# Optimization experiments

Measured on AMD Instinct MI355X. Metric: run time of the kernel, lower is better.

## Reference

```python
import jax, jax.numpy as jnp
import numpy as np

B, D, H, Z, E = 2048, 1024, 1024, 256, 64


def setup_inputs() -> dict:
    key = jax.random.key(0)
    ks = jax.random.split(key, 16)
    s = lambda k, shape, std=0.02: jax.random.normal(k, shape, dtype=jnp.float32) * std
    return {
        "x": jax.random.normal(ks[0], (B, D), dtype=jnp.float32),
        "h0": jax.random.normal(ks[1], (B, H), dtype=jnp.float32),
        "c0": jax.random.normal(ks[2], (B, H), dtype=jnp.float32),
        "hhat0": jax.random.normal(ks[3], (B, Z), dtype=jnp.float32),
        "chat0": jax.random.normal(ks[4], (B, Z), dtype=jnp.float32),
        "hweight": s(ks[5], (Z + H + D, 4 * Z)),
        "hbias": jnp.zeros((4 * Z,), jnp.float32),
        "zweight_h": s(ks[6], (Z, 4 * E), 0.01),
        "zweight_x": s(ks[7], (Z, 4 * E), 0.01),
        "zweight_b": s(ks[8], (Z, 4 * E), 0.01),
        "zbias_h": jnp.ones((4 * E,), jnp.float32),
        "zbias_x": jnp.ones((4 * E,), jnp.float32),
        # stacked in gate order (i, g, f, o), matching the torch cat order
        "dweight_h": jnp.full((4, E, H), 0.1 / E, jnp.float32),
        "dweight_x": jnp.full((4, E, H), 0.1 / E, jnp.float32),
        "dweight_b": s(ks[9], (4, E, H), 0.01),
        "weight": s(ks[10], (H + D, 4 * H)),
        "bias": jnp.zeros((4 * H,), jnp.float32),
    }


def reference(x, h0, c0, hhat0, chat0, hweight, hbias,
              zweight_h, zweight_x, zweight_b, zbias_h, zbias_x,
              dweight_h, dweight_x, dweight_b, weight, bias):
    # ---- hyper LSTM cell ----
    hcat = jnp.concatenate([hhat0, h0, x], axis=1)                 # [B, Z+H+D]
    hg = hcat @ hweight + hbias                                    # [B, 4Z]
    i_h, g_h, f_h, o_h = jnp.split(hg, 4, axis=1)
    chat1 = jax.nn.sigmoid(f_h) * chat0 + jax.nn.sigmoid(i_h) * jnp.tanh(g_h)
    hhat1 = jax.nn.sigmoid(o_h) * jnp.tanh(chat1)                  # [B, Z]

    # ---- embeddings z (gate order i, g, f, o) ----
    z_h = (hhat1 @ zweight_h + zbias_h).reshape(-1, 4, E)          # [B,4,E]
    z_x = (hhat1 @ zweight_x + zbias_x).reshape(-1, 4, E)
    z_b = (hhat1 @ zweight_b).reshape(-1, 4, E)

    # ---- per-gate modulation vectors d_y* : [B,4,H] -> [B,4H] ----
    d_yh = jnp.einsum('bge,geh->bgh', z_h, dweight_h).reshape(-1, 4 * H)
    d_yx = jnp.einsum('bge,geh->bgh', z_x, dweight_x).reshape(-1, 4 * H)
    d_yb = jnp.einsum('bge,geh->bgh', z_b, dweight_b).reshape(-1, 4 * H)

    # ---- main LSTM with hypernetwork modulation ----
    gates = jnp.concatenate([h0, x], axis=1) @ weight              # [B, 4H]
    gates = gates * d_yh * d_yx + d_yb + bias
    i_g, g_g, f_g, o_g = jnp.split(gates, 4, axis=1)
    c1 = jax.nn.sigmoid(f_g) * c0 + jax.nn.sigmoid(i_g) * jnp.tanh(g_g)
    h1 = jax.nn.sigmoid(o_g) * jnp.tanh(c1)
    return (h1, c1, hhat1, chat1)
```

## Files before the change

kernel.cpp:

```cpp
#include <hip/hip_runtime.h>
#include <hip/hip_bf16.h>
#include <math.h>


typedef __attribute__((ext_vector_type(8))) short bf16x8;
typedef __attribute__((ext_vector_type(4))) float f32x4;
typedef unsigned short u16;

__device__ __forceinline__ u16 f2b(float f) {
  union { float f; unsigned u; } v; v.f = f;
  unsigned r = v.u + 0x7fffu + ((v.u >> 16) & 1u);
  return (u16)(r >> 16);
}
__device__ __forceinline__ float b2f(u16 b) {
  union { unsigned u; float f; } v; v.u = ((unsigned)b) << 16; return v.f;
}
__device__ __forceinline__ float sigm(float x) { return 1.f / (1.f + __expf(-x)); }

#define GLL16(gsrc, ldst)                                                      \
  __builtin_amdgcn_global_load_lds(                                            \
      (const __attribute__((address_space(1))) void*)(gsrc),                   \
      (__attribute__((address_space(3))) void*)(ldst), 16, 0, 0)

__global__ void k_prep(const float* __restrict__ hhat0, const float* __restrict__ h0,
                       const float* __restrict__ x, const float* __restrict__ weight,
                       const float* __restrict__ hweight,
                       const float* __restrict__ zw_h, const float* __restrict__ zw_x,
                       const float* __restrict__ zw_b, const float* __restrict__ dw_h,
                       const float* __restrict__ dw_x, const float* __restrict__ dw_b,
                       u16* __restrict__ hcatb, u16* __restrict__ bt,
                       u16* __restrict__ zwT, u16* __restrict__ dwT) {
  __shared__ float tile[32][66];
  int bid = blockIdx.x;
  const int t = threadIdx.x;
  if (bid < 4608) {
    int i = bid * 256 + t;
    int b = i / 576, c4 = i % 576;
    const float* src;
    if (c4 < 64)       src = hhat0 + (long)b * 256 + c4 * 4;
    else if (c4 < 320) src = h0 + (long)b * 1024 + (c4 - 64) * 4;
    else               src = x + (long)b * 1024 + (c4 - 320) * 4;
    float4 v = *(const float4*)src;
    ushort4 o = {f2b(v.x), f2b(v.y), f2b(v.z), f2b(v.w)};
    *(ushort4*)&hcatb[(long)b * 2304 + c4 * 4] = o;
    return;
  }
  bid -= 4608;
  if (bid < 5760) {
    const int n0 = (bid % 160) * 32, k0 = (bid / 160) * 64;
    if (n0 < 4096 && k0 < 256) return;
    const float* src; int C, sc0, sr0;
    if (n0 >= 4096) { src = hweight; C = 1024; sc0 = n0 - 4096; sr0 = k0; }
    else            { src = weight;  C = 4096; sc0 = n0;        sr0 = k0 - 256; }
    #pragma unroll
    for (int p = 0; p < 8; ++p) {
      int c = t & 31, r = (t >> 5) + 8 * p;
      tile[c][r] = src[(long)(sr0 + r) * C + sc0 + c];
    }
    __syncthreads();
    #pragma unroll
    for (int p = 0; p < 2; ++p) {
      int kc = t & 15, cl = (t >> 4) + 16 * p;
      ushort4 o = {f2b(tile[cl][4 * kc]), f2b(tile[cl][4 * kc + 1]),
                   f2b(tile[cl][4 * kc + 2]), f2b(tile[cl][4 * kc + 3])};
      *(ushort4*)&bt[(long)(n0 + cl) * 2304 + k0 + 4 * kc] = o;
    }
    return;
  }
  bid -= 5760;
  const int zi = bid >> 5, bx = bid & 31;
  const float* src; u16* dst; int R, C;
  if (zi < 3) {
    src = (zi == 0) ? zw_h : (zi == 1) ? zw_x : zw_b;
    dst = zwT + (long)zi * 65536; R = 256; C = 256;
  } else {
    int s = zi - 3, tt = s >> 2, g = s & 3;
    src = ((tt == 0) ? dw_h : (tt == 1) ? dw_x : dw_b) + (long)g * 65536;
    dst = dwT + (long)s * 65536; R = 64; C = 1024;
  }
  const int nct = C / 32;
  const int c0 = (bx % nct) * 32, r0 = (bx / nct) * 64;
  #pragma unroll
  for (int p = 0; p < 8; ++p) {
    int c = t & 31, r = (t >> 5) + 8 * p;
    tile[c][r] = src[(long)(r0 + r) * C + c0 + c];
  }
  __syncthreads();
  #pragma unroll
  for (int p = 0; p < 2; ++p) {
    int kc = t & 15, cl = (t >> 4) + 16 * p;
    ushort4 o = {f2b(tile[cl][4 * kc]), f2b(tile[cl][4 * kc + 1]),
                 f2b(tile[cl][4 * kc + 2]), f2b(tile[cl][4 * kc + 3])};
    *(ushort4*)&dst[(long)(c0 + cl) * R + r0 + 4 * kc] = o;
  }
}

__global__ __launch_bounds__(512, 4)
void k_gemm_main(const u16* __restrict__ A, const u16* __restrict__ Bt,
                 float* __restrict__ hgbuf, u16* __restrict__ grawb) {
  constexpr int K = 2304, BK = 32;
  __shared__ __align__(16) u16 sA[128 * BK];
  __shared__ __align__(16) u16 sB[128 * BK];
  const int m0 = blockIdx.y * 128, n0 = blockIdx.x * 128;
  const int kstart = (n0 < 4096) ? 256 : 0;
  const int tid = threadIdx.x, wave = tid >> 6, lane = tid & 63;
  const int quad = lane >> 4, lrow = lane & 15;
  const int wm = (wave >> 2) * 64, wn = (wave & 3) * 32;

  const int sl = tid * 16;
  const int srow = sl >> 6;
  const int sq = (((sl & 63) >> 4) - (srow >> 1)) & 3;
  const long aoff = ((long)(m0 + srow) * K) * 2 + sq * 16;
  const long boff = ((long)(n0 + srow) * K) * 2 + sq * 16;

  const f32x4 vz = {0.f, 0.f, 0.f, 0.f};
  f32x4 acc[4][2];
  #pragma unroll
  for (int i = 0; i < 4; ++i)
    #pragma unroll
    for (int j = 0; j < 2; ++j) acc[i][j] = vz;

  for (int k0 = kstart; k0 < K; k0 += BK) {
    GLL16((const char*)A + aoff + (long)k0 * 2, (char*)sA + wave * 1024);
    GLL16((const char*)Bt + boff + (long)k0 * 2, (char*)sB + wave * 1024);
    __syncthreads();
    bf16x8 af[4], bf[2];
    #pragma unroll
    for (int i = 0; i < 4; ++i) {
      int row = wm + i * 16 + lrow;
      af[i] = *(const bf16x8*)((const char*)sA + row * 64 + (((quad + (row >> 1)) & 3) << 4));
    }
    #pragma unroll
    for (int j = 0; j < 2; ++j) {
      int row = wn + j * 16 + lrow;
      bf[j] = *(const bf16x8*)((const char*)sB + row * 64 + (((quad + (row >> 1)) & 3) << 4));
    }
    #pragma unroll
    for (int i = 0; i < 4; ++i)
      #pragma unroll
      for (int j = 0; j < 2; ++j)
        acc[i][j] = __builtin_amdgcn_mfma_f32_16x16x32_bf16(af[i], bf[j], acc[i][j], 0, 0, 0);
    __syncthreads();
  }
  #pragma unroll
  for (int i = 0; i < 4; ++i) {
    #pragma unroll
    for (int j = 0; j < 2; ++j) {
      #pragma unroll
      for (int r = 0; r < 4; ++r) {
        int row = m0 + wm + i * 16 + quad * 4 + r;
        int col = n0 + wn + j * 16 + lrow;
        float v = acc[i][j][r];
        if (col < 4096) grawb[(long)row * 4096 + col] = f2b(v);
        else            hgbuf[(long)row * 1024 + (col - 4096)] = v;
      }
    }
  }
}

__global__ __launch_bounds__(256, 2)
void k_gemm_z(const u16* __restrict__ A, const u16* __restrict__ Bt,
              const float* __restrict__ zbh, const float* __restrict__ zbx,
              u16* __restrict__ zbout) {
  constexpr int K = 256, BK = 32;
  __shared__ __align__(16) u16 sA[64 * BK];
  __shared__ __align__(16) u16 sB[128 * BK];
  const int m0 = blockIdx.y * 64, n0 = blockIdx.x * 128;
  const int tid = threadIdx.x, wave = tid >> 6, lane = tid & 63;
  const int quad = lane >> 4, lrow = lane & 15;
  const int wm = (wave >> 1) * 32, wn = (wave & 1) * 64;

  const int sl = tid * 16;
  const int arow = sl >> 6;
  const int aq = (((sl & 63) >> 4) - (arow >> 1)) & 3;
  const long aoff = ((long)(m0 + arow) * K) * 2 + aq * 16;

  const f32x4 vz = {0.f, 0.f, 0.f, 0.f};
  f32x4 acc[2][4];
  #pragma unroll
  for (int i = 0; i < 2; ++i)
    #pragma unroll
    for (int j = 0; j < 4; ++j) acc[i][j] = vz;

  for (int k0 = 0; k0 < K; k0 += BK) {
    GLL16((const char*)A + aoff + (long)k0 * 2, (char*)sA + wave * 1024);
    #pragma unroll
    for (int c = 0; c < 2; ++c) {
      int l = c * 4096 + sl;
      int row = l >> 6;
      int q = (((l & 63) >> 4) - (row >> 1)) & 3;
      const char* g = (const char*)Bt + ((long)(n0 + row) * K + k0) * 2 + q * 16;
      GLL16(g, (char*)sB + c * 4096 + wave * 1024);
    }
    __syncthreads();
    bf16x8 af[2], bf[4];
    #pragma unroll
    for (int i = 0; i < 2; ++i) {
      int row = wm + i * 16 + lrow;
      af[i] = *(const bf16x8*)((const char*)sA + row * 64 + (((quad + (row >> 1)) & 3) << 4));
    }
    #pragma unroll
    for (int j = 0; j < 4; ++j) {
      int row = wn + j * 16 + lrow;
      bf[j] = *(const bf16x8*)((const char*)sB + row * 64 + (((quad + (row >> 1)) & 3) << 4));
    }
    #pragma unroll
    for (int i = 0; i < 2; ++i)
      #pragma unroll
      for (int j = 0; j < 4; ++j)
        acc[i][j] = __builtin_amdgcn_mfma_f32_16x16x32_bf16(af[i], bf[j], acc[i][j], 0, 0, 0);
    __syncthreads();
  }
  #pragma unroll
  for (int i = 0; i < 2; ++i) {
    #pragma unroll
    for (int j = 0; j < 4; ++j) {
      #pragma unroll
      for (int r = 0; r < 4; ++r) {
        int row = m0 + wm + i * 16 + quad * 4 + r;
        int col = n0 + wn + j * 16 + lrow;
        float v = acc[i][j][r] + ((col < 256) ? zbh[col] : (col < 512) ? zbx[col - 256] : 0.f);
        zbout[(long)row * 768 + col] = f2b(v);
      }
    }
  }
}

__global__ void k_hyper_act(const float* __restrict__ hgbuf, const float* __restrict__ hbias,
                            const float* __restrict__ chat0,
                            float* __restrict__ chat1, float* __restrict__ hhat1,
                            u16* __restrict__ hhat1b) {
  int idx = blockIdx.x * 256 + threadIdx.x;
  int b = idx >> 8, zc = idx & 255;
  const float* row = hgbuf + (long)b * 1024;
  float ih = row[zc] + hbias[zc];
  float gh = row[256 + zc] + hbias[256 + zc];
  float fh = row[512 + zc] + hbias[512 + zc];
  float oh = row[768 + zc] + hbias[768 + zc];
  float c = sigm(fh) * chat0[idx] + sigm(ih) * tanhf(gh);
  float h = sigm(oh) * tanhf(c);
  chat1[idx] = c;
  hhat1[idx] = h;
  hhat1b[idx] = f2b(h);
}

__global__ __launch_bounds__(256, 2)
void k_dmod_lstm(const u16* __restrict__ z, const u16* __restrict__ dwT,
                 const u16* __restrict__ grawb, const float* __restrict__ bias,
                 const float* __restrict__ c0, float* __restrict__ h1,
                 float* __restrict__ c1) {
  __shared__ __align__(16) u16 sZ[64 * 192];
  __shared__ __align__(16) u16 sW[3 * 64 * 64];
  const int m0 = blockIdx.y * 64;
  const int hc0 = blockIdx.x * 64;
  const int tid = threadIdx.x, wave = tid >> 6, lane = tid & 63;
  const int quad = lane >> 4, lrow = lane & 15;
  const int wm = (wave >> 1) * 32, wn = (wave & 1) * 32;
  const f32x4 vz4 = {0.f, 0.f, 0.f, 0.f};

  f32x4 pcar[2][2];
  f32x4 ccar[2][2];

  #pragma unroll
  for (int g = 0; g < 4; ++g) {
    #pragma unroll
    for (int c = 0; c < 6; ++c) {
      int l = c * 4096 + tid * 16;
      int ci = l >> 4, row = ci / 24, p = ci - row * 24;
      int q = p + 72 - row; q -= (q / 24) * 24;
      int tt = q >> 3, e16 = q & 7;
      const char* gz = (const char*)z + (long)(m0 + row) * 1536 + tt * 512 + g * 128 + e16 * 16;
      GLL16(gz, (char*)sZ + c * 4096 + wave * 1024);
      int t2 = l >> 13, rw = (l & 8191) >> 7, p2 = (l >> 4) & 7;
      int q2 = (p2 - rw) & 7;
      const char* gw = (const char*)dwT + (long)((t2 * 4 + g) * 1024 + hc0 + rw) * 128 + q2 * 16;
      GLL16(gw, (char*)sW + c * 4096 + wave * 1024);
    }
    __syncthreads();
    f32x4 aH[2][2], aX[2][2], aB[2][2];
    #pragma unroll
    for (int i = 0; i < 2; ++i)
      #pragma unroll
      for (int j = 0; j < 2; ++j) { aH[i][j] = vz4; aX[i][j] = vz4; aB[i][j] = vz4; }
    #pragma unroll
    for (int kk = 0; kk < 2; ++kk) {
      bf16x8 za[3][2], wb[3][2];
      #pragma unroll
      for (int t = 0; t < 3; ++t) {
        #pragma unroll
        for (int i = 0; i < 2; ++i) {
          int row = wm + i * 16 + lrow;
          int q0 = t * 8 + kk * 4 + quad;
          int ph = q0 + row; ph -= (ph / 24) * 24;
          za[t][i] = *(const bf16x8*)((const char*)sZ + row * 384 + ph * 16);
        }
        #pragma unroll
        for (int j = 0; j < 2; ++j) {
          int row = wn + j * 16 + lrow;
          int q0 = kk * 4 + quad;
          int ph = (q0 + row) & 7;
          wb[t][j] = *(const bf16x8*)((const char*)sW + t * 8192 + row * 128 + ph * 16);
        }
      }
      #pragma unroll
      for (int i = 0; i < 2; ++i)
        #pragma unroll
        for (int j = 0; j < 2; ++j) {
          aH[i][j] = __builtin_amdgcn_mfma_f32_16x16x32_bf16(za[0][i], wb[0][j], aH[i][j], 0, 0, 0);
          aX[i][j] = __builtin_amdgcn_mfma_f32_16x16x32_bf16(za[1][i], wb[1][j], aX[i][j], 0, 0, 0);
          aB[i][j] = __builtin_amdgcn_mfma_f32_16x16x32_bf16(za[2][i], wb[2][j], aB[i][j], 0, 0, 0);
        }
    }
    __syncthreads();
    #pragma unroll
    for (int i = 0; i < 2; ++i) {
      #pragma unroll
      for (int j = 0; j < 2; ++j) {
        #pragma unroll
        for (int r = 0; r < 4; ++r) {
          int row = m0 + wm + i * 16 + quad * 4 + r;
          int col = wn + j * 16 + lrow;
          float gr = b2f(grawb[(long)row * 4096 + g * 1024 + hc0 + col]);
          float v = gr * aH[i][j][r] * aX[i][j][r] + aB[i][j][r] + bias[g * 1024 + hc0 + col];
          long idx = (long)row * 1024 + hc0 + col;
          if (g == 0) pcar[i][j][r] = sigm(v);
          else if (g == 1) pcar[i][j][r] *= tanhf(v);
          else if (g == 2) {
            float cc = sigm(v) * c0[idx] + pcar[i][j][r];
            ccar[i][j][r] = cc;
            c1[idx] = cc;
          } else {
            h1[idx] = sigm(v) * tanhf(ccar[i][j][r]);
          }
        }
      }
    }
  }
}


extern "C" void kernel_launch(void* const* d_in, const int* in_sizes, int n_in,
                              void* d_out, int out_size, void* d_ws, size_t ws_size,
                              hipStream_t stream) {
  const float* x      = (const float*)d_in[0];
  const float* h0     = (const float*)d_in[1];
  const float* c0     = (const float*)d_in[2];
  const float* hhat0  = (const float*)d_in[3];
  const float* chat0  = (const float*)d_in[4];
  const float* hweight= (const float*)d_in[5];
  const float* hbias  = (const float*)d_in[6];
  const float* zw_h   = (const float*)d_in[7];
  const float* zw_x   = (const float*)d_in[8];
  const float* zw_b   = (const float*)d_in[9];
  const float* zb_h   = (const float*)d_in[10];
  const float* zb_x   = (const float*)d_in[11];
  const float* dw_h   = (const float*)d_in[12];
  const float* dw_x   = (const float*)d_in[13];
  const float* dw_b   = (const float*)d_in[14];
  const float* weight = (const float*)d_in[15];
  const float* bias   = (const float*)d_in[16];
  float* out = (float*)d_out;

  char* w = (char*)d_ws;
  auto take = [&](size_t bytes) { char* p = w; w += (bytes + 255) & ~(size_t)255; return p; };
  u16*   hcatb  = (u16*)take(2048ull * 2304 * 2);
  u16*   btc    = (u16*)take(5120ull * 2304 * 2);
  u16*   zwT    = (u16*)take(768ull * 256 * 2);
  u16*   dwT    = (u16*)take(12ull * 1024 * 64 * 2);
  u16*   grawb  = (u16*)take(2048ull * 4096 * 2);
  float* hgbuf  = (float*)take(2048ull * 1024 * 4);
  u16*   hhat1b = (u16*)take(2048ull * 256 * 2);
  u16*   zb16   = (u16*)take(2048ull * 768 * 2);

  float* h1_o    = out;
  float* c1_o    = out + 2048 * 1024;
  float* hhat1_o = out + 2 * 2048 * 1024;
  float* chat1_o = out + 2 * 2048 * 1024 + 2048 * 256;

  k_prep<<<4608 + 5760 + 480, 256, 0, stream>>>(
      hhat0, h0, x, weight, hweight, zw_h, zw_x, zw_b, dw_h, dw_x, dw_b,
      hcatb, btc, zwT, dwT);

  k_gemm_main<<<dim3(40, 16), 512, 0, stream>>>(hcatb, btc, hgbuf, grawb);

  k_hyper_act<<<2048, 256, 0, stream>>>(hgbuf, hbias, chat0, chat1_o, hhat1_o, hhat1b);

  k_gemm_z<<<dim3(6, 32), 256, 0, stream>>>(hhat1b, zwT, zb_h, zb_x, zb16);

  k_dmod_lstm<<<dim3(16, 32), 256, 0, stream>>>(zb16, dwT, grawb, bias, c0, h1_o, c1_o);
}
```

Measured before the change: 230.6 us.

## Double-buffer LDS tiles and widen K step to 64 in main GEMM

The main bf16 GEMM now uses a K step of 64 instead of 32 and keeps two LDS buffers for A and B. The next tile's global-to-LDS loads are issued before the current tile is computed, and only one barrier is used per step. This is meant to hide global load latency and halve the number of loop iterations and barriers. In exchange, LDS use per block rises from 16KB to 64KB, which may lower occupancy under the 512-thread, 4-block launch bounds. The swizzle is also changed to an 8-way XOR over 128-byte rows.

```diff
diff --git a/kernel.cpp b/kernel.cpp
--- a/kernel.cpp
+++ b/kernel.cpp
@@ -98,20 +98,23 @@
 __global__ __launch_bounds__(512, 4)
 void k_gemm_main(const u16* __restrict__ A, const u16* __restrict__ Bt,
                  float* __restrict__ hgbuf, u16* __restrict__ grawb) {
-  constexpr int K = 2304, BK = 32;
-  __shared__ __align__(16) u16 sA[128 * BK];
-  __shared__ __align__(16) u16 sB[128 * BK];
+  constexpr int K = 2304, BK = 64;
+  __shared__ __align__(16) u16 sA[2][128 * BK];
+  __shared__ __align__(16) u16 sB[2][128 * BK];
   const int m0 = blockIdx.y * 128, n0 = blockIdx.x * 128;
   const int kstart = (n0 < 4096) ? 256 : 0;
   const int tid = threadIdx.x, wave = tid >> 6, lane = tid & 63;
   const int quad = lane >> 4, lrow = lane & 15;
   const int wm = (wave >> 2) * 64, wn = (wave & 3) * 32;
 
-  const int sl = tid * 16;
-  const int srow = sl >> 6;
-  const int sq = (((sl & 63) >> 4) - (srow >> 1)) & 3;
-  const long aoff = ((long)(m0 + srow) * K) * 2 + sq * 16;
-  const long boff = ((long)(n0 + srow) * K) * 2 + sq * 16;
+  const int la = tid * 16;
+  const int rowa = la >> 7, qa = (((la >> 4) & 7) - rowa) & 7;
+  const int lb = 8192 + tid * 16;
+  const int rowb = lb >> 7, qb = (((lb >> 4) & 7) - rowb) & 7;
+  const long aoff0 = ((long)(m0 + rowa) * K + qa * 8) * 2;
+  const long aoff1 = ((long)(m0 + rowb) * K + qb * 8) * 2;
+  const long boff0 = ((long)(n0 + rowa) * K + qa * 8) * 2;
+  const long boff1 = ((long)(n0 + rowb) * K + qb * 8) * 2;
 
   const f32x4 vz = {0.f, 0.f, 0.f, 0.f};
   f32x4 acc[4][2];
@@ -120,28 +123,52 @@
     #pragma unroll
     for (int j = 0; j < 2; ++j) acc[i][j] = vz;
 
-  for (int k0 = kstart; k0 < K; k0 += BK) {
-    GLL16((const char*)A + aoff + (long)k0 * 2, (char*)sA + wave * 1024);
-    GLL16((const char*)Bt + boff + (long)k0 * 2, (char*)sB + wave * 1024);
-    __syncthreads();
-    bf16x8 af[4], bf[2];
+  auto stage = [&](int d, int k0) {
+    GLL16((const char*)A + aoff0 + (long)k0 * 2, (char*)sA[d] + wave * 1024);
+    GLL16((const char*)A + aoff1 + (long)k0 * 2, (char*)sA[d] + 8192 + wave * 1024);
+    GLL16((const char*)Bt + boff0 + (long)k0 * 2, (char*)sB[d] + wave * 1024);
+    GLL16((const char*)Bt + boff1 + (long)k0 * 2, (char*)sB[d] + 8192 + wave * 1024);
+  };
+
+  auto compute = [&](int d) {
+    bf16x8 af[4][2], bf[2][2];
+    const char* pA = (const char*)sA[d];
+    const char* pB = (const char*)sB[d];
     #pragma unroll
     for (int i = 0; i < 4; ++i) {
       int row = wm + i * 16 + lrow;
-      af[i] = *(const bf16x8*)((const char*)sA + row * 64 + (((quad + (row >> 1)) & 3) << 4));
+      const char* base = pA + row * 128;
+      af[i][0] = *(const bf16x8*)(base + (((quad + row) & 7) << 4));
+      af[i][1] = *(const bf16x8*)(base + (((4 + quad + row) & 7) << 4));
     }
     #pragma unroll
     for (int j = 0; j < 2; ++j) {
       int row = wn + j * 16 + lrow;
-      bf[j] = *(const bf16x8*)((const char*)sB + row * 64 + (((quad + (row >> 1)) & 3) << 4));
-    }
-    #pragma unroll
-    for (int i = 0; i < 4; ++i)
-      #pragma unroll
-      for (int j = 0; j < 2; ++j)
-        acc[i][j] = __builtin_amdgcn_mfma_f32_16x16x32_bf16(af[i], bf[j], acc[i][j], 0, 0, 0);
-    __syncthreads();
-  }
+      const char* base = pB + row * 128;
+      bf[j][0] = *(const bf16x8*)(base + (((quad + row) & 7) << 4));
+      bf[j][1] = *(const bf16x8*)(base + (((4 + quad + row) & 7) << 4));
+    }
+    #pragma unroll
+    for (int kk = 0; kk < 2; ++kk)
+      #pragma unroll
+      for (int i = 0; i < 4; ++i)
+        #pragma unroll
+        for (int j = 0; j < 2; ++j)
+          acc[i][j] = __builtin_amdgcn_mfma_f32_16x16x32_bf16(af[i][kk], bf[j][kk], acc[i][j], 0, 0, 0);
+  };
+
+  const int nsteps = (K - kstart) >> 6;
+  stage(0, kstart);
+  __syncthreads();
+  int k0 = kstart + BK;
+  for (int s = 0; s < nsteps - 1; ++s, k0 += BK) {
+    const int d = s & 1;
+    stage(d ^ 1, k0);
+    compute(d);
+    __syncthreads();
+  }
+  compute((nsteps - 1) & 1);
+
   #pragma unroll
   for (int i = 0; i < 4; ++i) {
     #pragma unroll
```

Result: slower. 252.7 us (+9.6%).
